# Kernel optimization log

Measured on AMD Instinct MI355X. Metric: run time of the kernel, lower is better.

## Reference

```python
import jax, jax.numpy as jnp
from jax import lax
import numpy as np

B, T, V, C = 32, 2048, 21, 3
S0, S1, S2, S3, S4 = 16, 32, 64, 128, 128
A, NC = 4, 4
H = V * S0
TM1 = T - 1
BN_EPS = 1e-5
GROUPS = [([0, 9, 10, 11, 12], [0.1, 0.1, 0.2, 0.2, 0.4]),
          ([13, 14, 15, 16], [0.1, 0.2, 0.3, 0.4]),
          ([17, 18, 19, 20], [0.1, 0.2, 0.3, 0.4]),
          ([1, 2, 3, 4], [0.1, 0.2, 0.3, 0.4]),
          ([5, 6, 7, 8], [0.1, 0.2, 0.3, 0.4])]


def qeuler_zyx(q):
    # q: (..., 4) = (w, x, y, z); QuaterNet qeuler with order='zyx', epsilon=0
    q0, q1, q2, q3 = q[..., 0], q[..., 1], q[..., 2], q[..., 3]
    ex = jnp.arctan2(2 * (q0 * q1 - q2 * q3), 1 - 2 * (q1 * q1 + q2 * q2))
    ey = jnp.arcsin(jnp.clip(2 * (q1 * q3 + q0 * q2), -1.0, 1.0))
    ez = jnp.arctan2(2 * (q0 * q3 - q1 * q2), 1 - 2 * (q2 * q2 + q3 * q3))
    return jnp.stack([ex, ey, ez], axis=-1)


def conv1d(x, w, b, pad):
    # x: (B, Cin, L), w: (Cout, Cin, K)
    y = lax.conv_general_dilated(x, w, (1,), [(pad, pad)],
                                 dimension_numbers=('NCH', 'OIH', 'NCH'))
    return y + b[None, :, None]


def gru_layer(x, h0, Wih, Whh, bih, bhh):
    # x: (B, T, In), h0: (B, H); PyTorch GRU cell math
    gx_all = jnp.einsum('bti,gi->btg', x, Wih) + bih  # (B, T, 3H)

    def step(hc, gx):
        gh = hc @ Whh.T + bhh
        xr, xz, xn = jnp.split(gx, 3, axis=-1)
        hr, hz, hn = jnp.split(gh, 3, axis=-1)
        r = jax.nn.sigmoid(xr + hr)
        z = jax.nn.sigmoid(xz + hz)
        n = jnp.tanh(xn + r * hn)
        hn_new = (1 - z) * n + z * hc
        return hn_new, hn_new

    hT, ys = lax.scan(step, h0, jnp.swapaxes(gx_all, 0, 1))
    return jnp.swapaxes(ys, 0, 1), hT


def _forward(x_diffs, h, Wih0, Whh0, bih0, bhh0, Wih1, Whh1, bih1, bhh1,
             W2, b2, W3, b3, W3z, b3z, Wza, bza, W4, b4, W5, b5,
             bn_gamma, bn_beta, Wc, bc):
    b = x_diffs.shape[0]
    xd = jnp.transpose(x_diffs, (0, 2, 1))                 # (B, T-1, V*4)
    q = xd.reshape(b, TM1, V, 4)
    e = qeuler_zyx(q)                                      # (B, T-1, V, 3)
    # F.normalize default dim=1 (time axis), eps=1e-12
    nrm = jnp.sqrt(jnp.sum(e * e, axis=1, keepdims=True))
    e = e / jnp.maximum(nrm, 1e-12)
    x = e.reshape(b, TM1, V * C)
    y0, h0T = gru_layer(x, h[0], Wih0, Whh0, bih0, bhh0)
    y1, h1T = gru_layer(y0, h[1], Wih1, Whh1, bih1, bhh1)  # (B, T-1, H)
    hT = jnp.stack([h0T, h1T])                             # (2, B, H)
    # split hidden into V per-joint slices of size S0 -> (V, B, S0, T-1)
    xj = y1.reshape(b, TM1, V, S0).transpose(2, 0, 3, 1)
    yj = jax.nn.elu(jax.vmap(lambda xv, wv, bv: conv1d(xv, wv, bv, 2))(xj, W2, b2))  # (V,B,S1,T-1)

    def agg(idxs, wts):
        return jnp.einsum('k,kbct->bct', jnp.asarray(wts, yj.dtype), yj[jnp.asarray(idxs)])

    gs = [jax.nn.elu(conv1d(agg(i, w), W3[k], b3[k], 1)) for k, (i, w) in enumerate(GROUPS)]
    z_in = 0.12 * gs[0] + 0.22 * (gs[1] + gs[2] + gs[3] + gs[4])
    z = jax.nn.elu(conv1d(z_in, W3z, b3z, 1))              # (B, S2, T-1)
    affs = jax.nn.elu(conv1d(z, Wza, bza, 1))              # (B, A, T-1)
    lbl = jax.nn.elu(conv1d(affs, W4, b4, 0))              # (B, S3, T-1)
    lbl = jax.nn.elu(jnp.einsum('bct,dc->btd', lbl, W5) + b5)  # (B, T-1, S4)
    # eval-mode BatchNorm1d(T-1) over channel dim 1 (running mean 0, var 1)
    scale = bn_gamma / jnp.sqrt(1.0 + BN_EPS)
    lbl = lbl * scale[None, :, None] + bn_beta[None, :, None]
    logits = jnp.einsum('btd,cd->btc', lbl, Wc) + bc       # (B, T-1, NC)
    labels = jax.nn.sigmoid(logits)
    return jnp.transpose(affs, (0, 2, 1)), labels, hT


def setup_inputs() -> dict:
    key = jax.random.key(0)
    ks = jax.random.split(key, 16)
    n = lambda k, shp, sc=0.05: jax.random.normal(k, shp, jnp.float32) * sc
    return {
        'x_pose': n(ks[0], (B, V * C, TM1), 1.0),
        'x_diffs': n(ks[1], (B, V * 4, TM1), 1.0),
        'x_affs': n(ks[2], (B, A, TM1), 1.0),
        'h': jnp.zeros((2, B, H), jnp.float32),
        'Wih0': n(ks[3], (3 * H, V * C)), 'Whh0': n(ks[4], (3 * H, H)),
        'bih0': jnp.zeros((3 * H,), jnp.float32), 'bhh0': jnp.zeros((3 * H,), jnp.float32),
        'Wih1': n(ks[5], (3 * H, H)), 'Whh1': n(ks[6], (3 * H, H)),
        'bih1': jnp.zeros((3 * H,), jnp.float32), 'bhh1': jnp.zeros((3 * H,), jnp.float32),
        'W2': n(ks[7], (V, S1, S0, 5)), 'b2': jnp.zeros((V, S1), jnp.float32),
        'W3': n(ks[8], (5, S2, S1, 3)), 'b3': jnp.zeros((5, S2), jnp.float32),
        'W3z': n(ks[9], (S2, S2, 3)), 'b3z': jnp.zeros((S2,), jnp.float32),
        'Wza': n(ks[10], (A, S2, 3)), 'bza': jnp.zeros((A,), jnp.float32),
        'W4': n(ks[11], (S3, A, 1)), 'b4': jnp.zeros((S3,), jnp.float32),
        'W5': n(ks[12], (S4, S3)), 'b5': jnp.zeros((S4,), jnp.float32),
        'bn_gamma': jnp.ones((TM1,), jnp.float32), 'bn_beta': jnp.zeros((TM1,), jnp.float32),
        'Wc': n(ks[13], (NC, S4)), 'bc': jnp.zeros((NC,), jnp.float32),
    }


def reference(x_pose, x_diffs, x_affs, h, Wih0, Whh0, bih0, bhh0, Wih1, Whh1,
              bih1, bhh1, W2, b2, W3, b3, W3z, b3z, Wza, bza, W4, b4, W5, b5,
              bn_gamma, bn_beta, Wc, bc):
    # x_pose and x_affs are unused in the original forward
    return _forward(x_diffs, h, Wih0, Whh0, bih0, bhh0, Wih1, Whh1, bih1, bhh1,
                    W2, b2, W3, b3, W3z, b3z, Wza, bza, W4, b4, W5, b5,
                    bn_gamma, bn_beta, Wc, bc)
```

## Files before the change

### kernel.cpp

```cpp
#include <hip/hip_runtime.h>
#include <math.h>

#define TM1 2047
#define NB 32
#define NV 21
#define HH 336
#define G3 1008
#define CH 256
#define FLG_STRIDE 32

__device__ __forceinline__ float elu_f(float x){ return x > 0.f ? x : (expf(x) - 1.f); }
__device__ __forceinline__ float sigm_f(float x){ return 1.f / (1.f + expf(-x)); }

__global__ __launch_bounds__(256) void k_euler(const float* __restrict__ xd, float* __restrict__ xout){
  int b = blockIdx.x / NV, v = blockIdx.x % NV;
  const float* q = xd + ((size_t)b * 84 + 4 * v) * TM1;
  float ex[8], ey[8], ez[8];
  float sx = 0.f, sy = 0.f, sz = 0.f;
#pragma unroll
  for(int it = 0; it < 8; ++it){
    int t = threadIdx.x + it * 256;
    float e0 = 0.f, e1 = 0.f, e2 = 0.f;
    if(t < TM1){
      float q0 = q[t], q1 = q[TM1 + t], q2 = q[2 * TM1 + t], q3 = q[3 * TM1 + t];
      e0 = atan2f(2.f * (q0 * q1 - q2 * q3), 1.f - 2.f * (q1 * q1 + q2 * q2));
      float s = 2.f * (q1 * q3 + q0 * q2);
      s = fminf(1.f, fmaxf(-1.f, s));
      e1 = asinf(s);
      e2 = atan2f(2.f * (q0 * q3 - q1 * q2), 1.f - 2.f * (q2 * q2 + q3 * q3));
    }
    ex[it] = e0; ey[it] = e1; ez[it] = e2;
    sx += e0 * e0; sy += e1 * e1; sz += e2 * e2;
  }
  __shared__ float rb[3][256];
  rb[0][threadIdx.x] = sx; rb[1][threadIdx.x] = sy; rb[2][threadIdx.x] = sz;
  __syncthreads();
  if(threadIdx.x < 3){
    float s = 0.f;
    for(int i = 0; i < 256; ++i) s += rb[threadIdx.x][i];
    rb[threadIdx.x][0] = 1.f / fmaxf(sqrtf(s), 1e-12f);
  }
  __syncthreads();
  float i0 = rb[0][0], i1 = rb[1][0], i2 = rb[2][0];
  float* xo = xout + ((size_t)b * 63 + 3 * v) * TM1;
#pragma unroll
  for(int it = 0; it < 8; ++it){
    int t = threadIdx.x + it * 256;
    if(t < TM1){
      xo[t]            = ex[it] * i0;
      xo[TM1 + t]      = ey[it] * i1;
      xo[2 * TM1 + t]  = ez[it] * i2;
    }
  }
}

template<int K, int KC, bool XKT>
__global__ __launch_bounds__(256) void k_gx(const float* __restrict__ xin, int xrows, int xbase,
                                            const float* __restrict__ Wih, const float* __restrict__ bih,
                                            float* __restrict__ gx, int gxrows, int tbase){
  __shared__ float ys[KC][68];
  __shared__ float wsm[KC][68];
  int trel0 = blockIdx.x * 64;
  int g0 = blockIdx.y * 64;
  int b  = blockIdx.z;
  int gi = threadIdx.x & 15, ti = threadIdx.x >> 4;
  float acc[4][4];
#pragma unroll
  for(int a = 0; a < 4; ++a)
#pragma unroll
    for(int c = 0; c < 4; ++c) acc[a][c] = 0.f;

  for(int k0 = 0; k0 < K; k0 += KC){
    if(XKT){
      for(int idx = threadIdx.x; idx < KC * 64; idx += 256){
        int kk = idx >> 6, tt = idx & 63; int t = tbase + trel0 + tt;
        ys[kk][tt] = (t < TM1) ? xin[((size_t)b * K + k0 + kk) * TM1 + t] : 0.f;
      }
    } else {
      for(int idx = threadIdx.x; idx < 64 * KC; idx += 256){
        int tt = idx / KC, kk = idx % KC; int t = tbase + trel0 + tt;
        ys[kk][tt] = (t < TM1) ? xin[((size_t)b * xrows + (t - xbase)) * K + k0 + kk] : 0.f;
      }
    }
    for(int idx = threadIdx.x; idx < 64 * KC; idx += 256){
      int gg = idx / KC, kk = idx % KC; int g = g0 + gg;
      wsm[kk][gg] = (g < G3) ? Wih[(size_t)g * K + k0 + kk] : 0.f;
    }
    __syncthreads();
    int klim = (K - k0 < KC) ? (K - k0) : KC;
    for(int kk = 0; kk < klim; ++kk){
      float4 xv = *(const float4*)&ys[kk][ti * 4];
      float4 wv = *(const float4*)&wsm[kk][gi * 4];
      float xa[4] = {xv.x, xv.y, xv.z, xv.w};
      float wa[4] = {wv.x, wv.y, wv.z, wv.w};
#pragma unroll
      for(int a = 0; a < 4; ++a)
#pragma unroll
        for(int c = 0; c < 4; ++c) acc[a][c] += xa[a] * wa[c];
    }
    __syncthreads();
  }
#pragma unroll
  for(int a = 0; a < 4; ++a){
    int trel = trel0 + ti * 4 + a;
    int t = tbase + trel;
    if(t >= TM1) continue;
    int g = g0 + gi * 4;
    float* gp = gx + ((size_t)b * gxrows + trel) * G3;
    if(g + 3 < G3){
      float4 o;
      o.x = acc[a][0] + bih[g];   o.y = acc[a][1] + bih[g+1];
      o.z = acc[a][2] + bih[g+2]; o.w = acc[a][3] + bih[g+3];
      *(float4*)&gp[g] = o;
    } else {
#pragma unroll
      for(int c = 0; c < 4; ++c){ if(g + c < G3) gp[g + c] = acc[a][c] + bih[g + c]; }
    }
  }
}

#define GU 8
#define UU 42
#define SCAN_T 512

__global__ __launch_bounds__(SCAN_T) void k_scan(const float* __restrict__ Whh, const float* __restrict__ bhh,
    const float* __restrict__ gx, int gxrows,
    float* hb0, float* hb1,
    float* __restrict__ yout, int yrows, int ybase,
    float* __restrict__ hT, int* flg_base, int t0, int tn){
  int ug = blockIdx.x >> 4, pr = blockIdx.x & 15;
  int u0 = ug * UU, b0 = pr * 2;
  int tid = threadIdx.x;
  int* flg = flg_base + pr * (GU * FLG_STRIDE);
  __shared__ float hl[2][HH];
  __shared__ float part[3 * UU][4][2];

  int r = tid >> 2, kq = tid & 3;
  bool act = (tid < 3 * UU * 4);
  float w[84];
  if(act){
    int rglob = (r / UU) * HH + u0 + (r % UU);
    const float* wp = Whh + (size_t)rglob * HH + kq * 84;
#pragma unroll
    for(int j = 0; j < 84; ++j) w[j] = wp[j];
  }
  bool comb = (tid < 2 * UU);
  int cu = tid % UU, cb = tid / UU;
  float bh_r = 0.f, bh_z = 0.f, bh_n = 0.f;
  const float* gxp = gx;
  if(comb){
    bh_r = bhh[u0 + cu]; bh_z = bhh[HH + u0 + cu]; bh_n = bhh[2 * HH + u0 + cu];
    gxp = gx + ((size_t)(b0 + cb) * gxrows) * G3 + u0 + cu;
  }
  float* hcur = ((t0 & 1) == 0) ? hb0 : hb1;
  float* hnxt = ((t0 & 1) == 0) ? hb1 : hb0;
  for(int ti = 0; ti < tn; ++ti){
    int t = t0 + ti;
    float gr = 0.f, gz = 0.f, gn = 0.f;
    if(comb){
      const float* gp = gxp + (size_t)ti * G3;
      gr = gp[0]; gz = gp[HH]; gn = gp[2 * HH];
    }
    if(t > 0 && tid < GU){
      while(__hip_atomic_load(flg + tid * FLG_STRIDE, __ATOMIC_RELAXED, __HIP_MEMORY_SCOPE_AGENT) < t)
        __builtin_amdgcn_s_sleep(1);
    }
    __syncthreads();
    for(int idx = tid; idx < 2 * HH; idx += SCAN_T){
      int bs = (idx >= HH), k = idx - bs * HH;
      hl[bs][k] = __hip_atomic_load(&hcur[(size_t)(b0 + bs) * HH + k],
                                    __ATOMIC_RELAXED, __HIP_MEMORY_SCOPE_AGENT);
    }
    __syncthreads();
    if(act){
      float a0 = 0.f, a1 = 0.f;
#pragma unroll
      for(int jj = 0; jj < 21; ++jj){
        float4 h0 = *(const float4*)&hl[0][kq * 84 + jj * 4];
        float4 h1 = *(const float4*)&hl[1][kq * 84 + jj * 4];
        a0 += w[jj*4+0]*h0.x + w[jj*4+1]*h0.y + w[jj*4+2]*h0.z + w[jj*4+3]*h0.w;
        a1 += w[jj*4+0]*h1.x + w[jj*4+1]*h1.y + w[jj*4+2]*h1.z + w[jj*4+3]*h1.w;
      }
      part[r][kq][0] = a0; part[r][kq][1] = a1;
    }
    __syncthreads();
    float hnew = 0.f;
    if(comb){
      float ghr = part[cu][0][cb] + part[cu][1][cb] + part[cu][2][cb] + part[cu][3][cb] + bh_r;
      float ghz = part[UU+cu][0][cb] + part[UU+cu][1][cb] + part[UU+cu][2][cb] + part[UU+cu][3][cb] + bh_z;
      float ghn = part[2*UU+cu][0][cb] + part[2*UU+cu][1][cb] + part[2*UU+cu][2][cb] + part[2*UU+cu][3][cb] + bh_n;
      float rg = sigm_f(gr + ghr);
      float zg = sigm_f(gz + ghz);
      float ng = tanhf(gn + rg * ghn);
      float hold = hl[cb][u0 + cu];
      hnew = (1.f - zg) * ng + zg * hold;
      __hip_atomic_store(&hnxt[(size_t)(b0 + cb) * HH + u0 + cu], hnew,
                         __ATOMIC_RELAXED, __HIP_MEMORY_SCOPE_AGENT);
    }
    __syncthreads();
    if(tid == 0)
      __hip_atomic_store(flg + ug * FLG_STRIDE, t + 1,
                         __ATOMIC_RELAXED, __HIP_MEMORY_SCOPE_AGENT);
    if(comb){
      yout[((size_t)(b0 + cb) * yrows + (t - ybase)) * HH + u0 + cu] = hnew;
      if(t == TM1 - 1) hT[(size_t)(b0 + cb) * HH + u0 + cu] = hnew;
    }
    float* tmp = hcur; hcur = hnxt; hnxt = tmp;
  }
}

__global__ __launch_bounds__(256) void k_head(const float* __restrict__ y1,
   const float* __restrict__ W2, const float* __restrict__ b2,
   const float* __restrict__ W3, const float* __restrict__ b3,
   const float* __restrict__ W3z, const float* __restrict__ b3z,
   const float* __restrict__ Wza, const float* __restrict__ bza,
   const float* __restrict__ W4, const float* __restrict__ b4,
   const float* __restrict__ W5, const float* __restrict__ b5,
   const float* __restrict__ gmm, const float* __restrict__ bet,
   const float* __restrict__ Wc, const float* __restrict__ bc,
   float* __restrict__ out_affs, float* __restrict__ out_lab){
  __shared__ float sm[11402];
  float* aggp = sm;
  float* zinp = sm + 6080;
  float* zzp  = sm + 8384;
  float* ystp = sm + 10560;
  float* affp = sm + 11274;
  float* lblA = sm + 6080;
  float* lgpp = sm;
  int t0 = blockIdx.x * 32;
  int b  = blockIdx.y;
  int tid = threadIdx.x;

  for(int i = tid; i < 6080; i += 256) aggp[i] = 0.f;
  for(int i = tid; i < 2304; i += 256) zinp[i] = 0.f;
  __syncthreads();

  const int   vg_[21] = {0,3,3,3,3,4,4,4,4,0,0,0,0,1,1,1,1,2,2,2,2};
  const float vw_[21] = {0.1f,0.1f,0.2f,0.3f,0.4f,0.1f,0.2f,0.3f,0.4f,
                         0.1f,0.2f,0.2f,0.4f,0.1f,0.2f,0.3f,0.4f,0.1f,0.2f,0.3f,0.4f};

  {
    int o = tid >> 3, q = tid & 7;
    for(int v = 0; v < NV; ++v){
      for(int idx = tid; idx < 42 * 16; idx += 256){
        int ts = idx >> 4, i = idx & 15; int t = t0 - 5 + ts;
        ystp[ts * 17 + i] = (t >= 0 && t < TM1) ? y1[((size_t)b * TM1 + t) * HH + v * 16 + i] : 0.f;
      }
      __syncthreads();
      int g = vg_[v]; float wv = vw_[v];
      const float* wp = W2 + v * 2560 + o * 80;
      float acc5[5];
      float bias = b2[v * 32 + o];
#pragma unroll
      for(int j = 0; j < 5; ++j) acc5[j] = bias;
#pragma unroll
      for(int i = 0; i < 16; ++i){
        float w0 = wp[i*5+0], w1 = wp[i*5+1], w2v = wp[i*5+2], w3v = wp[i*5+3], w4v = wp[i*5+4];
#pragma unroll
        for(int j = 0; j < 5; ++j){
          int ts = q * 5 + j;
          if(ts < 38){
            acc5[j] += w0*ystp[ts*17+i] + w1*ystp[(ts+1)*17+i] + w2v*ystp[(ts+2)*17+i]
                     + w3v*ystp[(ts+3)*17+i] + w4v*ystp[(ts+4)*17+i];
          }
        }
      }
#pragma unroll
      for(int j = 0; j < 5; ++j){
        int ts = q * 5 + j;
        if(ts < 38){
          int t = t0 - 3 + ts;
          if(t >= 0 && t < TM1) aggp[(g * 32 + o) * 38 + ts] += wv * elu_f(acc5[j]);
        }
      }
      __syncthreads();
    }
  }

  {
    int c = tid >> 2, q = tid & 3;
    for(int k5 = 0; k5 < 5; ++k5){
      float coef = (k5 == 0) ? 0.12f : 0.22f;
      const float* wp = W3 + k5 * 6144 + c * 96;
      float accv[9];
      float bias = b3[k5 * 64 + c];
#pragma unroll
      for(int j = 0; j < 9; ++j) accv[j] = bias;
      for(int i = 0; i < 32; ++i){
        float w0 = wp[i*3+0], w1 = wp[i*3+1], w2v = wp[i*3+2];
        const float* ap = &aggp[(k5 * 32 + i) * 38 + q * 9];
#pragma unroll
        for(int j = 0; j < 9; ++j)
          accv[j] += w0*ap[j] + w1*ap[j+1] + w2v*ap[j+2];
      }
      __syncthreads();
#pragma unroll
      for(int j = 0; j < 9; ++j){
        int ts = q * 9 + j;
        int t = t0 - 2 + ts;
        if(t >= 0 && t < TM1) zinp[c * 36 + ts] += coef * elu_f(accv[j]);
      }
      __syncthreads();
    }
  }

  {
    int c = tid >> 2, q = tid & 3;
    const float* wp = W3z + c * 192;
    float accv[9];
    float bias = b3z[c];
#pragma unroll
    for(int j = 0; j < 9; ++j) accv[j] = bias;
    for(int i = 0; i < 64; ++i){
      float w0 = wp[i*3+0], w1 = wp[i*3+1], w2v = wp[i*3+2];
      const float* zp = &zinp[i * 36 + q * 9];
#pragma unroll
      for(int j = 0; j < 9; ++j)
        accv[j] += w0*zp[j] + w1*zp[j+1] + w2v*zp[j+2];
    }
    __syncthreads();
#pragma unroll
    for(int j = 0; j < 9; ++j){
      int ts = q * 9 + j;
      if(ts < 34){
        int t = t0 - 1 + ts;
        zzp[c * 34 + ts] = (t >= 0 && t < TM1) ? elu_f(accv[j]) : 0.f;
      }
    }
    __syncthreads();
  }

  if(tid < 128){
    int a = tid >> 5, tt = tid & 31;
    const float* wp = Wza + a * 192;
    float acc = bza[a];
    for(int i = 0; i < 64; ++i){
      const float* zp = &zzp[i * 34 + tt];
      acc += wp[i*3+0]*zp[0] + wp[i*3+1]*zp[1] + wp[i*3+2]*zp[2];
    }
    float av = elu_f(acc);
    affp[a * 32 + tt] = av;
    int t = t0 + tt;
    if(t < TM1) out_affs[((size_t)b * TM1 + t) * 4 + a] = av;
  }
  __syncthreads();

  for(int idx = tid; idx < 4096; idx += 256){
    int d = idx >> 5, tt = idx & 31;
    float acc = b4[d] + W4[d*4+0]*affp[tt] + W4[d*4+1]*affp[32+tt]
              + W4[d*4+2]*affp[64+tt] + W4[d*4+3]*affp[96+tt];
    lblA[idx] = elu_f(acc);
  }
  __syncthreads();

  {
    int tt = tid >> 3, dg = tid & 7;
    float l2[16];
#pragma unroll
    for(int dd = 0; dd < 16; ++dd) l2[dd] = b5[dg * 16 + dd];
    for(int cc = 0; cc < 128; ++cc){
      float xv = lblA[cc * 32 + tt];
#pragma unroll
      for(int dd = 0; dd < 16; ++dd)
        l2[dd] += W5[(dg * 16 + dd) * 128 + cc] * xv;
    }
    int t = t0 + tt;
    float sc = 0.f, bb = 0.f;
    if(t < TM1){ sc = gmm[t] * rsqrtf(1.f + 1e-5f); bb = bet[t]; }
    float lg[4] = {0.f, 0.f, 0.f, 0.f};
#pragma unroll
    for(int dd = 0; dd < 16; ++dd){
      int d = dg * 16 + dd;
      float val = elu_f(l2[dd]) * sc + bb;
#pragma unroll
      for(int c = 0; c < 4; ++c) lg[c] += Wc[c * 128 + d] * val;
    }
    __syncthreads();
#pragma unroll
    for(int c = 0; c < 4; ++c) lgpp[(tt * 8 + dg) * 4 + c] = lg[c];
  }
  __syncthreads();
  if(tid < 128){
    int tt = tid >> 2, c = tid & 3;
    float s = bc[c];
#pragma unroll
    for(int dg = 0; dg < 8; ++dg) s += lgpp[(tt * 8 + dg) * 4 + c];
    int ta = t0 + tt;
    if(ta < TM1) out_lab[((size_t)b * TM1 + ta) * 4 + c] = sigm_f(s);
  }
}

extern "C" void kernel_launch(void* const* d_in, const int* in_sizes, int n_in,
                              void* d_out, int out_size, void* d_ws, size_t ws_size,
                              hipStream_t stream){
  (void)in_sizes; (void)n_in; (void)out_size; (void)ws_size;
  const float* x_diffs = (const float*)d_in[1];
  const float* h_init  = (const float*)d_in[3];
  const float* Wih0 = (const float*)d_in[4];
  const float* Whh0 = (const float*)d_in[5];
  const float* bih0 = (const float*)d_in[6];
  const float* bhh0 = (const float*)d_in[7];
  const float* Wih1 = (const float*)d_in[8];
  const float* Whh1 = (const float*)d_in[9];
  const float* bih1 = (const float*)d_in[10];
  const float* bhh1 = (const float*)d_in[11];
  const float* W2  = (const float*)d_in[12];
  const float* b2  = (const float*)d_in[13];
  const float* W3  = (const float*)d_in[14];
  const float* b3  = (const float*)d_in[15];
  const float* W3z = (const float*)d_in[16];
  const float* b3z = (const float*)d_in[17];
  const float* Wza = (const float*)d_in[18];
  const float* bza = (const float*)d_in[19];
  const float* W4  = (const float*)d_in[20];
  const float* b4  = (const float*)d_in[21];
  const float* W5  = (const float*)d_in[22];
  const float* b5  = (const float*)d_in[23];
  const float* gmm = (const float*)d_in[24];
  const float* bet = (const float*)d_in[25];
  const float* Wc  = (const float*)d_in[26];
  const float* bc  = (const float*)d_in[27];
  float* out = (float*)d_out;

  float* ws   = (float*)d_ws;
  float* x_ws = ws;
  float* y1   = x_ws + 4126752;
  float* gxb  = y1 + 22009344;
  float* y0c  = gxb + 8257536;
  float* hb   = y0c + 2752512;
  int*   flg  = (int*)(hb + 43008);

  float* out_affs = out;
  float* out_lab  = out + (size_t)NB * TM1 * 4;
  float* hT0 = out + 2 * (size_t)NB * TM1 * 4;
  float* hT1 = hT0 + NB * HH;

  (void)hipMemsetAsync(flg, 0, 2 * 16 * GU * FLG_STRIDE * sizeof(int), stream);
  (void)hipMemcpyAsync(hb,               h_init,           NB * HH * sizeof(float), hipMemcpyDeviceToDevice, stream);
  (void)hipMemcpyAsync(hb + 2 * NB * HH, h_init + NB * HH, NB * HH * sizeof(float), hipMemcpyDeviceToDevice, stream);

  k_euler<<<dim3(NB * NV), 256, 0, stream>>>(x_diffs, x_ws);

  for(int c = 0; c < 8; ++c){
    int t0 = c * CH;
    int tn = (TM1 - t0 < CH) ? (TM1 - t0) : CH;
    int gtiles = (tn + 63) / 64;
    k_gx<63, 63, true><<<dim3(gtiles, 16, NB), 256, 0, stream>>>(
        x_ws, 0, 0, Wih0, bih0, gxb, CH, t0);
    k_scan<<<dim3(GU * 16), SCAN_T, 0, stream>>>(
        Whh0, bhh0, gxb, CH, hb, hb + NB * HH, y0c, CH, t0, hT0, flg, t0, tn);
    k_gx<336, 112, false><<<dim3(gtiles, 16, NB), 256, 0, stream>>>(
        y0c, CH, t0, Wih1, bih1, gxb, CH, t0);
    k_scan<<<dim3(GU * 16), SCAN_T, 0, stream>>>(
        Whh1, bhh1, gxb, CH, hb + 2 * NB * HH, hb + 3 * NB * HH, y1, TM1, 0, hT1,
        flg + 16 * GU * FLG_STRIDE, t0, tn);
  }

  k_head<<<dim3(64, NB), 256, 0, stream>>>(y1, W2, b2, W3, b3, W3z, b3z, Wza, bza,
                                           W4, b4, W5, b5, gmm, bet, Wc, bc,
                                           out_affs, out_lab);
}
```

Before: 14.72 ms.

## Fuse both GRU layers into one persistent wavefront-pipelined kernel with ring buffer

Replaces the chunked loop of input-projection GEMMs and per-layer scan kernels with one persistent kernel of 256 blocks. Half the blocks run layer 0 and half run layer 1, and the two layers are pipelined through a 256-step ring buffer of layer-0 outputs, coordinated by flags. Each step now computes the input projection inline from register-resident Wih weights, so the gx buffer and the separate GEMM launches go away. In exchange the per-step work and register pressure rise (wx[84] plus wh[84] in layer 1), and correctness depends on all 256 blocks being co-resident for the spin-waits.

```diff
diff --git a/kernel.cpp b/kernel.cpp
--- a/kernel.cpp
+++ b/kernel.cpp
@@ -6,8 +6,11 @@
 #define NV 21
 #define HH 336
 #define G3 1008
-#define CH 256
 #define FLG_STRIDE 32
+#define GU 8
+#define UU 42
+#define SCAN_T 512
+#define RING 256
 
 __device__ __forceinline__ float elu_f(float x){ return x > 0.f ? x : (expf(x) - 1.f); }
 __device__ __forceinline__ float sigm_f(float x){ return 1.f / (1.f + expf(-x)); }
@@ -54,158 +57,192 @@
   }
 }
 
-template<int K, int KC, bool XKT>
-__global__ __launch_bounds__(256) void k_gx(const float* __restrict__ xin, int xrows, int xbase,
-                                            const float* __restrict__ Wih, const float* __restrict__ bih,
-                                            float* __restrict__ gx, int gxrows, int tbase){
-  __shared__ float ys[KC][68];
-  __shared__ float wsm[KC][68];
-  int trel0 = blockIdx.x * 64;
-  int g0 = blockIdx.y * 64;
-  int b  = blockIdx.z;
-  int gi = threadIdx.x & 15, ti = threadIdx.x >> 4;
-  float acc[4][4];
-#pragma unroll
-  for(int a = 0; a < 4; ++a)
-#pragma unroll
-    for(int c = 0; c < 4; ++c) acc[a][c] = 0.f;
-
-  for(int k0 = 0; k0 < K; k0 += KC){
-    if(XKT){
-      for(int idx = threadIdx.x; idx < KC * 64; idx += 256){
-        int kk = idx >> 6, tt = idx & 63; int t = tbase + trel0 + tt;
-        ys[kk][tt] = (t < TM1) ? xin[((size_t)b * K + k0 + kk) * TM1 + t] : 0.f;
-      }
-    } else {
-      for(int idx = threadIdx.x; idx < 64 * KC; idx += 256){
-        int tt = idx / KC, kk = idx % KC; int t = tbase + trel0 + tt;
-        ys[kk][tt] = (t < TM1) ? xin[((size_t)b * xrows + (t - xbase)) * K + k0 + kk] : 0.f;
-      }
-    }
-    for(int idx = threadIdx.x; idx < 64 * KC; idx += 256){
-      int gg = idx / KC, kk = idx % KC; int g = g0 + gg;
-      wsm[kk][gg] = (g < G3) ? Wih[(size_t)g * K + k0 + kk] : 0.f;
-    }
-    __syncthreads();
-    int klim = (K - k0 < KC) ? (K - k0) : KC;
-    for(int kk = 0; kk < klim; ++kk){
-      float4 xv = *(const float4*)&ys[kk][ti * 4];
-      float4 wv = *(const float4*)&wsm[kk][gi * 4];
-      float xa[4] = {xv.x, xv.y, xv.z, xv.w};
-      float wa[4] = {wv.x, wv.y, wv.z, wv.w};
-#pragma unroll
-      for(int a = 0; a < 4; ++a)
-#pragma unroll
-        for(int c = 0; c < 4; ++c) acc[a][c] += xa[a] * wa[c];
-    }
-    __syncthreads();
-  }
-#pragma unroll
-  for(int a = 0; a < 4; ++a){
-    int trel = trel0 + ti * 4 + a;
-    int t = tbase + trel;
-    if(t >= TM1) continue;
-    int g = g0 + gi * 4;
-    float* gp = gx + ((size_t)b * gxrows + trel) * G3;
-    if(g + 3 < G3){
-      float4 o;
-      o.x = acc[a][0] + bih[g];   o.y = acc[a][1] + bih[g+1];
-      o.z = acc[a][2] + bih[g+2]; o.w = acc[a][3] + bih[g+3];
-      *(float4*)&gp[g] = o;
-    } else {
-#pragma unroll
-      for(int c = 0; c < 4; ++c){ if(g + c < G3) gp[g + c] = acc[a][c] + bih[g + c]; }
-    }
-  }
-}
-
-#define GU 8
-#define UU 42
-#define SCAN_T 512
-
-__global__ __launch_bounds__(SCAN_T) void k_scan(const float* __restrict__ Whh, const float* __restrict__ bhh,
-    const float* __restrict__ gx, int gxrows,
-    float* hb0, float* hb1,
-    float* __restrict__ yout, int yrows, int ybase,
-    float* __restrict__ hT, int* flg_base, int t0, int tn){
-  int ug = blockIdx.x >> 4, pr = blockIdx.x & 15;
+__global__ __launch_bounds__(SCAN_T) void k_fused(
+    const float* __restrict__ Whh0, const float* __restrict__ bhh0,
+    const float* __restrict__ Wih0, const float* __restrict__ bih0,
+    const float* __restrict__ Whh1, const float* __restrict__ bhh1,
+    const float* __restrict__ Wih1, const float* __restrict__ bih1,
+    const float* __restrict__ x_ws,
+    float* h0b, float* h1b, float* y0r, float* __restrict__ y1,
+    float* hT0, float* hT1, int* flg0, int* flg1){
+  int lay = blockIdx.x >> 7;
+  int idx = blockIdx.x & 127;
+  int ug = idx >> 4, pr = idx & 15;
   int u0 = ug * UU, b0 = pr * 2;
   int tid = threadIdx.x;
-  int* flg = flg_base + pr * (GU * FLG_STRIDE);
+  int* f0 = flg0 + pr * (GU * FLG_STRIDE);
+  int* f1 = flg1 + pr * (GU * FLG_STRIDE);
   __shared__ float hl[2][HH];
-  __shared__ float part[3 * UU][4][2];
+  __shared__ float yl[2][HH];
+  __shared__ float part_h[3*UU][4][2];
+  __shared__ float part_x[3*UU][4][2];
 
   int r = tid >> 2, kq = tid & 3;
   bool act = (tid < 3 * UU * 4);
-  float w[84];
-  if(act){
-    int rglob = (r / UU) * HH + u0 + (r % UU);
-    const float* wp = Whh + (size_t)rglob * HH + kq * 84;
-#pragma unroll
-    for(int j = 0; j < 84; ++j) w[j] = wp[j];
-  }
   bool comb = (tid < 2 * UU);
   int cu = tid % UU, cb = tid / UU;
-  float bh_r = 0.f, bh_z = 0.f, bh_n = 0.f;
-  const float* gxp = gx;
-  if(comb){
-    bh_r = bhh[u0 + cu]; bh_z = bhh[HH + u0 + cu]; bh_n = bhh[2 * HH + u0 + cu];
-    gxp = gx + ((size_t)(b0 + cb) * gxrows) * G3 + u0 + cu;
-  }
-  float* hcur = ((t0 & 1) == 0) ? hb0 : hb1;
-  float* hnxt = ((t0 & 1) == 0) ? hb1 : hb0;
-  for(int ti = 0; ti < tn; ++ti){
-    int t = t0 + ti;
-    float gr = 0.f, gz = 0.f, gn = 0.f;
+
+  if(lay == 0){
+    float wh[84], wx[16];
+    if(act){
+      int rglob = (r / UU) * HH + u0 + (r % UU);
+      const float* wp = Whh0 + (size_t)rglob * HH + kq * 84;
+#pragma unroll
+      for(int j = 0; j < 84; ++j) wh[j] = wp[j];
+      int k0 = kq * 16;
+      int xlen = 63 - k0; if(xlen > 16) xlen = 16;
+      const float* wq = Wih0 + (size_t)rglob * 63 + k0;
+#pragma unroll
+      for(int j = 0; j < 16; ++j) wx[j] = (j < xlen) ? wq[j] : 0.f;
+    }
+    float bh_r=0.f,bh_z=0.f,bh_n=0.f,bx_r=0.f,bx_z=0.f,bx_n=0.f;
     if(comb){
-      const float* gp = gxp + (size_t)ti * G3;
-      gr = gp[0]; gz = gp[HH]; gn = gp[2 * HH];
-    }
-    if(t > 0 && tid < GU){
-      while(__hip_atomic_load(flg + tid * FLG_STRIDE, __ATOMIC_RELAXED, __HIP_MEMORY_SCOPE_AGENT) < t)
-        __builtin_amdgcn_s_sleep(1);
-    }
-    __syncthreads();
-    for(int idx = tid; idx < 2 * HH; idx += SCAN_T){
-      int bs = (idx >= HH), k = idx - bs * HH;
-      hl[bs][k] = __hip_atomic_load(&hcur[(size_t)(b0 + bs) * HH + k],
-                                    __ATOMIC_RELAXED, __HIP_MEMORY_SCOPE_AGENT);
-    }
-    __syncthreads();
+      bh_r = bhh0[u0+cu]; bh_z = bhh0[HH+u0+cu]; bh_n = bhh0[2*HH+u0+cu];
+      bx_r = bih0[u0+cu]; bx_z = bih0[HH+u0+cu]; bx_n = bih0[2*HH+u0+cu];
+    }
+    if(tid == 508){ yl[0][63] = 0.f; yl[1][63] = 0.f; }
+    for(int t = 0; t < TM1; ++t){
+      if(t > 0 && tid < GU){
+        while(__hip_atomic_load(f0 + tid*FLG_STRIDE, __ATOMIC_RELAXED, __HIP_MEMORY_SCOPE_AGENT) < t)
+          __builtin_amdgcn_s_sleep(1);
+      }
+      if(t >= RING && tid >= 64 && tid < 64 + GU){
+        while(__hip_atomic_load(f1 + (tid-64)*FLG_STRIDE, __ATOMIC_RELAXED, __HIP_MEMORY_SCOPE_AGENT) < t - RING + 1)
+          __builtin_amdgcn_s_sleep(1);
+      }
+      __syncthreads();
+      float* hcur = h0b + (size_t)(t & 1) * NB * HH;
+      float* hnxt = h0b + (size_t)((t + 1) & 1) * NB * HH;
+      for(int i2 = tid; i2 < 2*HH; i2 += SCAN_T){
+        int bs = (i2 >= HH), k = i2 - bs*HH;
+        hl[bs][k] = __hip_atomic_load(&hcur[(size_t)(b0+bs)*HH + k],
+                                      __ATOMIC_RELAXED, __HIP_MEMORY_SCOPE_AGENT);
+      }
+      if(tid >= 384 && tid < 510){
+        int q = tid - 384; int cbx = q / 63, ch = q - cbx * 63;
+        yl[cbx][ch] = x_ws[((size_t)(b0+cbx)*63 + ch)*TM1 + t];
+      }
+      __syncthreads();
+      if(act){
+        float a0 = 0.f, a1 = 0.f;
+#pragma unroll
+        for(int jj = 0; jj < 21; ++jj){
+          float4 h0 = *(const float4*)&hl[0][kq*84 + jj*4];
+          float4 h1 = *(const float4*)&hl[1][kq*84 + jj*4];
+          a0 += wh[jj*4+0]*h0.x + wh[jj*4+1]*h0.y + wh[jj*4+2]*h0.z + wh[jj*4+3]*h0.w;
+          a1 += wh[jj*4+0]*h1.x + wh[jj*4+1]*h1.y + wh[jj*4+2]*h1.z + wh[jj*4+3]*h1.w;
+        }
+        part_h[r][kq][0] = a0; part_h[r][kq][1] = a1;
+        float c0 = 0.f, c1 = 0.f;
+        int k0 = kq * 16;
+#pragma unroll
+        for(int j = 0; j < 16; ++j){
+          c0 += wx[j] * yl[0][k0 + j];
+          c1 += wx[j] * yl[1][k0 + j];
+        }
+        part_x[r][kq][0] = c0; part_x[r][kq][1] = c1;
+      }
+      __syncthreads();
+      float hnew = 0.f;
+      if(comb){
+        float ghr = part_h[cu][0][cb]+part_h[cu][1][cb]+part_h[cu][2][cb]+part_h[cu][3][cb] + bh_r;
+        float gxr = part_x[cu][0][cb]+part_x[cu][1][cb]+part_x[cu][2][cb]+part_x[cu][3][cb] + bx_r;
+        float ghz = part_h[UU+cu][0][cb]+part_h[UU+cu][1][cb]+part_h[UU+cu][2][cb]+part_h[UU+cu][3][cb] + bh_z;
+        float gxz = part_x[UU+cu][0][cb]+part_x[UU+cu][1][cb]+part_x[UU+cu][2][cb]+part_x[UU+cu][3][cb] + bx_z;
+        float ghn = part_h[2*UU+cu][0][cb]+part_h[2*UU+cu][1][cb]+part_h[2*UU+cu][2][cb]+part_h[2*UU+cu][3][cb] + bh_n;
+        float gxn = part_x[2*UU+cu][0][cb]+part_x[2*UU+cu][1][cb]+part_x[2*UU+cu][2][cb]+part_x[2*UU+cu][3][cb] + bx_n;
+        float rg = sigm_f(gxr + ghr);
+        float zg = sigm_f(gxz + ghz);
+        float ng = tanhf(gxn + rg * ghn);
+        hnew = (1.f - zg) * ng + zg * hl[cb][u0 + cu];
+        __hip_atomic_store(&hnxt[(size_t)(b0+cb)*HH + u0+cu], hnew,
+                           __ATOMIC_RELAXED, __HIP_MEMORY_SCOPE_AGENT);
+        __hip_atomic_store(&y0r[((size_t)(b0+cb)*RING + (t & (RING-1)))*HH + u0+cu], hnew,
+                           __ATOMIC_RELAXED, __HIP_MEMORY_SCOPE_AGENT);
+      }
+      __syncthreads();
+      if(tid == 0)
+        __hip_atomic_store(f0 + ug*FLG_STRIDE, t + 1,
+                           __ATOMIC_RELAXED, __HIP_MEMORY_SCOPE_AGENT);
+      if(comb && t == TM1-1) hT0[(size_t)(b0+cb)*HH + u0+cu] = hnew;
+    }
+  } else {
+    float wh[84], wx[84];
     if(act){
-      float a0 = 0.f, a1 = 0.f;
-#pragma unroll
-      for(int jj = 0; jj < 21; ++jj){
-        float4 h0 = *(const float4*)&hl[0][kq * 84 + jj * 4];
-        float4 h1 = *(const float4*)&hl[1][kq * 84 + jj * 4];
-        a0 += w[jj*4+0]*h0.x + w[jj*4+1]*h0.y + w[jj*4+2]*h0.z + w[jj*4+3]*h0.w;
-        a1 += w[jj*4+0]*h1.x + w[jj*4+1]*h1.y + w[jj*4+2]*h1.z + w[jj*4+3]*h1.w;
-      }
-      part[r][kq][0] = a0; part[r][kq][1] = a1;
-    }
-    __syncthreads();
-    float hnew = 0.f;
+      int rglob = (r / UU) * HH + u0 + (r % UU);
+      const float* wp = Whh1 + (size_t)rglob * HH + kq * 84;
+      const float* wq = Wih1 + (size_t)rglob * HH + kq * 84;
+#pragma unroll
+      for(int j = 0; j < 84; ++j){ wh[j] = wp[j]; wx[j] = wq[j]; }
+    }
+    float bh_r=0.f,bh_z=0.f,bh_n=0.f,bx_r=0.f,bx_z=0.f,bx_n=0.f;
     if(comb){
-      float ghr = part[cu][0][cb] + part[cu][1][cb] + part[cu][2][cb] + part[cu][3][cb] + bh_r;
-      float ghz = part[UU+cu][0][cb] + part[UU+cu][1][cb] + part[UU+cu][2][cb] + part[UU+cu][3][cb] + bh_z;
-      float ghn = part[2*UU+cu][0][cb] + part[2*UU+cu][1][cb] + part[2*UU+cu][2][cb] + part[2*UU+cu][3][cb] + bh_n;
-      float rg = sigm_f(gr + ghr);
-      float zg = sigm_f(gz + ghz);
-      float ng = tanhf(gn + rg * ghn);
-      float hold = hl[cb][u0 + cu];
-      hnew = (1.f - zg) * ng + zg * hold;
-      __hip_atomic_store(&hnxt[(size_t)(b0 + cb) * HH + u0 + cu], hnew,
-                         __ATOMIC_RELAXED, __HIP_MEMORY_SCOPE_AGENT);
-    }
-    __syncthreads();
-    if(tid == 0)
-      __hip_atomic_store(flg + ug * FLG_STRIDE, t + 1,
-                         __ATOMIC_RELAXED, __HIP_MEMORY_SCOPE_AGENT);
-    if(comb){
-      yout[((size_t)(b0 + cb) * yrows + (t - ybase)) * HH + u0 + cu] = hnew;
-      if(t == TM1 - 1) hT[(size_t)(b0 + cb) * HH + u0 + cu] = hnew;
-    }
-    float* tmp = hcur; hcur = hnxt; hnxt = tmp;
+      bh_r = bhh1[u0+cu]; bh_z = bhh1[HH+u0+cu]; bh_n = bhh1[2*HH+u0+cu];
+      bx_r = bih1[u0+cu]; bx_z = bih1[HH+u0+cu]; bx_n = bih1[2*HH+u0+cu];
+    }
+    for(int t = 0; t < TM1; ++t){
+      if(tid < GU){
+        while(__hip_atomic_load(f0 + tid*FLG_STRIDE, __ATOMIC_RELAXED, __HIP_MEMORY_SCOPE_AGENT) < t + 1)
+          __builtin_amdgcn_s_sleep(1);
+      }
+      if(t > 0 && tid >= 64 && tid < 64 + GU){
+        while(__hip_atomic_load(f1 + (tid-64)*FLG_STRIDE, __ATOMIC_RELAXED, __HIP_MEMORY_SCOPE_AGENT) < t)
+          __builtin_amdgcn_s_sleep(1);
+      }
+      __syncthreads();
+      float* hcur = h1b + (size_t)(t & 1) * NB * HH;
+      float* hnxt = h1b + (size_t)((t + 1) & 1) * NB * HH;
+      for(int i2 = tid; i2 < 2*HH; i2 += SCAN_T){
+        int bs = (i2 >= HH), k = i2 - bs*HH;
+        hl[bs][k] = __hip_atomic_load(&hcur[(size_t)(b0+bs)*HH + k],
+                                      __ATOMIC_RELAXED, __HIP_MEMORY_SCOPE_AGENT);
+        yl[bs][k] = __hip_atomic_load(&y0r[((size_t)(b0+bs)*RING + (t & (RING-1)))*HH + k],
+                                      __ATOMIC_RELAXED, __HIP_MEMORY_SCOPE_AGENT);
+      }
+      __syncthreads();
+      if(act){
+        float a0=0.f, a1=0.f, c0=0.f, c1=0.f;
+#pragma unroll
+        for(int jj = 0; jj < 21; ++jj){
+          float4 h0 = *(const float4*)&hl[0][kq*84 + jj*4];
+          float4 h1 = *(const float4*)&hl[1][kq*84 + jj*4];
+          float4 y0v = *(const float4*)&yl[0][kq*84 + jj*4];
+          float4 y1v = *(const float4*)&yl[1][kq*84 + jj*4];
+          float w0 = wh[jj*4+0], w1 = wh[jj*4+1], w2 = wh[jj*4+2], w3 = wh[jj*4+3];
+          a0 += w0*h0.x + w1*h0.y + w2*h0.z + w3*h0.w;
+          a1 += w0*h1.x + w1*h1.y + w2*h1.z + w3*h1.w;
+          float v0 = wx[jj*4+0], v1 = wx[jj*4+1], v2 = wx[jj*4+2], v3 = wx[jj*4+3];
+          c0 += v0*y0v.x + v1*y0v.y + v2*y0v.z + v3*y0v.w;
+          c1 += v0*y1v.x + v1*y1v.y + v2*y1v.z + v3*y1v.w;
+        }
+        part_h[r][kq][0] = a0; part_h[r][kq][1] = a1;
+        part_x[r][kq][0] = c0; part_x[r][kq][1] = c1;
+      }
+      __syncthreads();
+      float hnew = 0.f;
+      if(comb){
+        float ghr = part_h[cu][0][cb]+part_h[cu][1][cb]+part_h[cu][2][cb]+part_h[cu][3][cb] + bh_r;
+        float gxr = part_x[cu][0][cb]+part_x[cu][1][cb]+part_x[cu][2][cb]+part_x[cu][3][cb] + bx_r;
+        float ghz = part_h[UU+cu][0][cb]+part_h[UU+cu][1][cb]+part_h[UU+cu][2][cb]+part_h[UU+cu][3][cb] + bh_z;
+        float gxz = part_x[UU+cu][0][cb]+part_x[UU+cu][1][cb]+part_x[UU+cu][2][cb]+part_x[UU+cu][3][cb] + bx_z;
+        float ghn = part_h[2*UU+cu][0][cb]+part_h[2*UU+cu][1][cb]+part_h[2*UU+cu][2][cb]+part_h[2*UU+cu][3][cb] + bh_n;
+        float gxn = part_x[2*UU+cu][0][cb]+part_x[2*UU+cu][1][cb]+part_x[2*UU+cu][2][cb]+part_x[2*UU+cu][3][cb] + bx_n;
+        float rg = sigm_f(gxr + ghr);
+        float zg = sigm_f(gxz + ghz);
+        float ng = tanhf(gxn + rg * ghn);
+        hnew = (1.f - zg) * ng + zg * hl[cb][u0 + cu];
+        __hip_atomic_store(&hnxt[(size_t)(b0+cb)*HH + u0+cu], hnew,
+                           __ATOMIC_RELAXED, __HIP_MEMORY_SCOPE_AGENT);
+      }
+      __syncthreads();
+      if(tid == 0)
+        __hip_atomic_store(f1 + ug*FLG_STRIDE, t + 1,
+                           __ATOMIC_RELAXED, __HIP_MEMORY_SCOPE_AGENT);
+      if(comb){
+        y1[((size_t)(b0+cb)*TM1 + t)*HH + u0+cu] = hnew;
+        if(t == TM1-1) hT1[(size_t)(b0+cb)*HH + u0+cu] = hnew;
+      }
+    }
   }
 }
 
@@ -425,10 +462,12 @@
   float* ws   = (float*)d_ws;
   float* x_ws = ws;
   float* y1   = x_ws + 4126752;
-  float* gxb  = y1 + 22009344;
-  float* y0c  = gxb + 8257536;
-  float* hb   = y0c + 2752512;
+  float* y0r  = y1 + 22009344;
+  float* hb   = y0r + 2752512;
   int*   flg  = (int*)(hb + 43008);
+
+  float* h0b = hb;
+  float* h1b = hb + 2 * NB * HH;
 
   float* out_affs = out;
   float* out_lab  = out + (size_t)NB * TM1 * 4;
@@ -436,25 +475,15 @@
   float* hT1 = hT0 + NB * HH;
 
   (void)hipMemsetAsync(flg, 0, 2 * 16 * GU * FLG_STRIDE * sizeof(int), stream);
-  (void)hipMemcpyAsync(hb,               h_init,           NB * HH * sizeof(float), hipMemcpyDeviceToDevice, stream);
-  (void)hipMemcpyAsync(hb + 2 * NB * HH, h_init + NB * HH, NB * HH * sizeof(float), hipMemcpyDeviceToDevice, stream);
+  (void)hipMemcpyAsync(h0b, h_init,           NB * HH * sizeof(float), hipMemcpyDeviceToDevice, stream);
+  (void)hipMemcpyAsync(h1b, h_init + NB * HH, NB * HH * sizeof(float), hipMemcpyDeviceToDevice, stream);
 
   k_euler<<<dim3(NB * NV), 256, 0, stream>>>(x_diffs, x_ws);
 
-  for(int c = 0; c < 8; ++c){
-    int t0 = c * CH;
-    int tn = (TM1 - t0 < CH) ? (TM1 - t0) : CH;
-    int gtiles = (tn + 63) / 64;
-    k_gx<63, 63, true><<<dim3(gtiles, 16, NB), 256, 0, stream>>>(
-        x_ws, 0, 0, Wih0, bih0, gxb, CH, t0);
-    k_scan<<<dim3(GU * 16), SCAN_T, 0, stream>>>(
-        Whh0, bhh0, gxb, CH, hb, hb + NB * HH, y0c, CH, t0, hT0, flg, t0, tn);
-    k_gx<336, 112, false><<<dim3(gtiles, 16, NB), 256, 0, stream>>>(
-        y0c, CH, t0, Wih1, bih1, gxb, CH, t0);
-    k_scan<<<dim3(GU * 16), SCAN_T, 0, stream>>>(
-        Whh1, bhh1, gxb, CH, hb + 2 * NB * HH, hb + 3 * NB * HH, y1, TM1, 0, hT1,
-        flg + 16 * GU * FLG_STRIDE, t0, tn);
-  }
+  k_fused<<<dim3(256), SCAN_T, 0, stream>>>(
+      Whh0, bhh0, Wih0, bih0, Whh1, bhh1, Wih1, bih1, x_ws,
+      h0b, h1b, y0r, y1, hT0, hT1,
+      flg, flg + 16 * GU * FLG_STRIDE);
 
   k_head<<<dim3(64, NB), 256, 0, stream>>>(y1, W2, b2, W3, b3, W3z, b3z, Wza, bza,
                                            W4, b4, W5, b5, gmm, bet, Wc, bc,
```

Result: slower. 18.28 ms (+24.2%).
